# Kernel optimization log

Measured on AMD Instinct MI355X. Metric: run time of the kernel, lower is better.

Reference implementation:

```python
import jax, jax.numpy as jnp
import numpy as np

DIM = 16
HID = 32

def setup_inputs() -> dict:
    key = jax.random.key(0)
    ks = jax.random.split(key, 5)
    B, S = 32768, 64
    x = jax.random.normal(ks[0], (B, S, DIM), dtype=jnp.float32)
    # LayerNorm params (torch defaults: weight=1, bias=0)
    ln_w = jnp.ones((DIM,), dtype=jnp.float32)
    ln_b = jnp.zeros((DIM,), dtype=jnp.float32)
    # Linear params, torch-style init scale ~ 1/sqrt(fan_in)
    w1 = jax.random.uniform(ks[1], (HID, DIM), jnp.float32, -1.0, 1.0) / np.sqrt(DIM)
    b1 = jax.random.uniform(ks[2], (HID,), jnp.float32, -1.0, 1.0) / np.sqrt(DIM)
    w2 = jax.random.uniform(ks[3], (DIM, HID), jnp.float32, -1.0, 1.0) / np.sqrt(HID)
    b2 = jax.random.uniform(ks[4], (DIM,), jnp.float32, -1.0, 1.0) / np.sqrt(HID)
    return {"x": x, "ln_w": ln_w, "ln_b": ln_b, "w1": w1, "b1": b1, "w2": w2, "b2": b2}

def _layernorm(x, w, b, eps=1e-5):
    mu = jnp.mean(x, axis=-1, keepdims=True)
    var = jnp.mean(jnp.square(x - mu), axis=-1, keepdims=True)
    return (x - mu) * jax.lax.rsqrt(var + eps) * w + b

def reference(x, ln_w, ln_b, w1, b1, w2, b2):
    h = _layernorm(x, ln_w, ln_b)
    h = jnp.einsum('bsd,hd->bsh', h, w1) + b1
    h = jax.nn.gelu(h, approximate=False)  # torch nn.GELU default is exact erf
    h = jnp.einsum('bsh,dh->bsd', h, w2) + b2
    return x + h
```

## Files before the change

kernel.cpp:

```cpp
#include <hip/hip_runtime.h>
#include <math.h>

#define DIM 16
#define HID 32

typedef float  f32x4  __attribute__((ext_vector_type(4)));
typedef short  bf16x8 __attribute__((ext_vector_type(8)));
typedef float  v2f    __attribute__((ext_vector_type(2)));

#define ROW_STRIDE_B 80
#define LDS_PER_WAVE (64 * ROW_STRIDE_B)

__device__ inline unsigned short f2bf(float f) {
    union { float f; unsigned u; } v; v.f = f;
    unsigned r = v.u + 0x7fffu + ((v.u >> 16) & 1u);
    return (unsigned short)(r >> 16);
}
__device__ inline unsigned packbf(float lo, float hi) {
    return (unsigned)f2bf(lo) | ((unsigned)f2bf(hi) << 16);
}

__device__ inline float gelu_erf(float x) {
    const float kInvSqrt2 = 0.70710678118654752f;
    float z  = x * kInvSqrt2;
    float az = fabsf(z);
    float t  = __builtin_amdgcn_rcpf(fmaf(0.3275911f, az, 1.0f));
    float e  = __expf(-az * az);
    float p  = fmaf(t, 1.061405429f, -1.453152027f);
    p = fmaf(t, p, 1.421413741f);
    p = fmaf(t, p, -0.284496736f);
    p = fmaf(t, p, 0.254829592f);
    p = p * t;
    float erf_abs = fmaf(-p, e, 1.0f);
    float erfv = copysignf(erf_abs, z);
    return 0.5f * x * (1.0f + erfv);
}

__global__ __launch_bounds__(256) void fused_ln_mlp_mfma(
    const float* __restrict__ x,
    const float* __restrict__ ln_w,
    const float* __restrict__ ln_b,
    const float* __restrict__ w1,
    const float* __restrict__ b1,
    const float* __restrict__ w2,
    const float* __restrict__ b2,
    float* __restrict__ out,
    int nrows)
{
    __shared__ __align__(16) unsigned char lds_all[4 * LDS_PER_WAVE];

    const int tid  = threadIdx.x;
    const int lane = tid & 63;
    const int wave = tid >> 6;
    const int q    = lane >> 4;
    const int c    = lane & 15;

    unsigned char* nbuf = lds_all + wave * LDS_PER_WAVE;
    const int rowbase = (blockIdx.x * 4 + wave) * 64;

    bf16x8 bW1[2];
    #pragma unroll
    for (int t = 0; t < 2; t++) {
        bf16x8 f = {0, 0, 0, 0, 0, 0, 0, 0};
        if (q < 2) {
            const float* wp = w1 + (c + 16 * t) * DIM + q * 8;
            #pragma unroll
            for (int j = 0; j < 8; j++)
                ((unsigned short*)&f)[j] = f2bf(wp[j]);
        }
        bW1[t] = f;
    }
    bf16x8 bW2;
    {
        const float* wp = w2 + c * HID + q * 8;
        #pragma unroll
        for (int j = 0; j < 8; j++)
            ((unsigned short*)&bW2)[j] = f2bf(wp[j]);
    }
    const float b1v0 = b1[c];
    const float b1v1 = b1[c + 16];
    const float b2v  = b2[c];

    const float* xr = x + (size_t)(rowbase + lane) * DIM;
    v2f xv2[8];
    {
        float4 t0 = *(const float4*)(xr + 0);
        float4 t1 = *(const float4*)(xr + 4);
        float4 t2 = *(const float4*)(xr + 8);
        float4 t3 = *(const float4*)(xr + 12);
        xv2[0] = (v2f){t0.x, t0.y}; xv2[1] = (v2f){t0.z, t0.w};
        xv2[2] = (v2f){t1.x, t1.y}; xv2[3] = (v2f){t1.z, t1.w};
        xv2[4] = (v2f){t2.x, t2.y}; xv2[5] = (v2f){t2.z, t2.w};
        xv2[6] = (v2f){t3.x, t3.y}; xv2[7] = (v2f){t3.z, t3.w};
    }
    v2f s = xv2[0] + xv2[1];
    s += xv2[2] + xv2[3];
    s += xv2[4] + xv2[5];
    s += xv2[6] + xv2[7];
    float mu = (s.x + s.y) * (1.0f / DIM);
    v2f mu2 = (v2f){mu, mu};
    v2f vs = (v2f){0.0f, 0.0f};
    #pragma unroll
    for (int i = 0; i < 8; i++) {
        v2f d = xv2[i] - mu2;
        vs = __builtin_elementwise_fma(d, d, vs);
    }
    float var = (vs.x + vs.y) * (1.0f / DIM);
    float a = __builtin_amdgcn_rsqf(var + 1e-5f);
    float cc = -mu * a;

    const v2f* lnw2 = (const v2f*)ln_w;
    const v2f* lnb2 = (const v2f*)ln_b;
    v2f a2 = (v2f){a, a};
    v2f c2 = (v2f){cc, cc};
    float xn[16];
    #pragma unroll
    for (int i = 0; i < 8; i++) {
        v2f xh = __builtin_elementwise_fma(xv2[i], a2, c2);
        v2f r  = __builtin_elementwise_fma(xh, lnw2[i], lnb2[i]);
        xn[2 * i]     = r.x;
        xn[2 * i + 1] = r.y;
    }

    {
        int4 w0, w1v, zz;
        w0.x  = packbf(xn[0],  xn[1]);  w0.y  = packbf(xn[2],  xn[3]);
        w0.z  = packbf(xn[4],  xn[5]);  w0.w  = packbf(xn[6],  xn[7]);
        w1v.x = packbf(xn[8],  xn[9]);  w1v.y = packbf(xn[10], xn[11]);
        w1v.z = packbf(xn[12], xn[13]); w1v.w = packbf(xn[14], xn[15]);
        zz.x = zz.y = zz.z = zz.w = 0;
        int4* rowp = (int4*)(nbuf + lane * ROW_STRIDE_B);
        rowp[0] = w0; rowp[1] = w1v; rowp[2] = zz; rowp[3] = zz;
    }
    asm volatile("s_waitcnt lgkmcnt(0)" ::: "memory");

    f32x4 accH[4][2];
    #pragma unroll
    for (int rc = 0; rc < 4; rc++) {
        const bf16x8 afrag =
            *(const bf16x8*)(nbuf + (rc * 16 + c) * ROW_STRIDE_B + q * 16);
        f32x4 z0 = {0.f, 0.f, 0.f, 0.f};
        f32x4 z1 = {0.f, 0.f, 0.f, 0.f};
        accH[rc][0] = __builtin_amdgcn_mfma_f32_16x16x32_bf16(afrag, bW1[0], z0, 0, 0, 0);
        accH[rc][1] = __builtin_amdgcn_mfma_f32_16x16x32_bf16(afrag, bW1[1], z1, 0, 0, 0);
    }
    asm volatile("s_waitcnt lgkmcnt(0)" ::: "memory");

    #pragma unroll
    for (int rc = 0; rc < 4; rc++) {
        #pragma unroll
        for (int t = 0; t < 2; t++) {
            #pragma unroll
            for (int r = 0; r < 4; r++) {
                float hv = accH[rc][t][r] + (t ? b1v1 : b1v0);
                float g  = gelu_erf(hv);
                *(unsigned short*)(nbuf + (rc * 16 + 4 * q + r) * ROW_STRIDE_B
                                        + (c + 16 * t) * 2) = f2bf(g);
            }
        }
    }
    asm volatile("s_waitcnt lgkmcnt(0)" ::: "memory");

    f32x4 accY[4];
    #pragma unroll
    for (int rc = 0; rc < 4; rc++) {
        const bf16x8 afrag =
            *(const bf16x8*)(nbuf + (rc * 16 + c) * ROW_STRIDE_B + q * 16);
        f32x4 z = {0.f, 0.f, 0.f, 0.f};
        accY[rc] = __builtin_amdgcn_mfma_f32_16x16x32_bf16(afrag, bW2, z, 0, 0, 0);
    }

    #pragma unroll
    for (int rc = 0; rc < 4; rc++) {
        #pragma unroll
        for (int r = 0; r < 4; r++) {
            int grow = rowbase + rc * 16 + 4 * q + r;
            float xres = x[(size_t)grow * DIM + c];
            out[(size_t)grow * DIM + c] = accY[rc][r] + b2v + xres;
        }
    }
}

extern "C" void kernel_launch(void* const* d_in, const int* in_sizes, int n_in,
                              void* d_out, int out_size, void* d_ws, size_t ws_size,
                              hipStream_t stream) {
    const float* x    = (const float*)d_in[0];
    const float* ln_w = (const float*)d_in[1];
    const float* ln_b = (const float*)d_in[2];
    const float* w1   = (const float*)d_in[3];
    const float* b1   = (const float*)d_in[4];
    const float* w2   = (const float*)d_in[5];
    const float* b2   = (const float*)d_in[6];
    float* out = (float*)d_out;

    int nrows = in_sizes[0] / DIM;
    int rows_per_block = 256;
    int grid = (nrows + rows_per_block - 1) / rows_per_block;

    fused_ln_mlp_mfma<<<grid, 256, 0, stream>>>(
        x, ln_w, ln_b, w1, b1, w2, b2, out, nrows);
}
```

Before: 254.3 us.

## Transpose MFMA operands for row-major outputs, vectorize GELU, bf16 packing and stores

Swaps the MFMA operand order so each lane's accumulator holds four consecutive hidden or output columns of a single row. This lets the GELU results be written to LDS as packed int2 stores and the residual read and output write use 16-byte vector accesses with nontemporal stores, in place of scalar scattered ones. It also replaces software bf16 rounding with the hardware v_cvt_pk_bf16_f32 instruction and rewrites GELU in packed two-wide form using exp2 directly. One LDS barrier stage is removed by fusing GELU into the first MFMA loop. The inline asm relies on the conversion instruction existing on this target.

```diff
diff --git a/kernel.cpp b/kernel.cpp
--- a/kernel.cpp
+++ b/kernel.cpp
@@ -16,24 +16,31 @@
     unsigned r = v.u + 0x7fffu + ((v.u >> 16) & 1u);
     return (unsigned short)(r >> 16);
 }
-__device__ inline unsigned packbf(float lo, float hi) {
-    return (unsigned)f2bf(lo) | ((unsigned)f2bf(hi) << 16);
+
+__device__ inline unsigned cvt_pk_bf16(float lo, float hi) {
+    unsigned r;
+    asm("v_cvt_pk_bf16_f32 %0, %1, %2" : "=v"(r) : "v"(lo), "v"(hi));
+    return r;
 }
 
-__device__ inline float gelu_erf(float x) {
-    const float kInvSqrt2 = 0.70710678118654752f;
-    float z  = x * kInvSqrt2;
-    float az = fabsf(z);
-    float t  = __builtin_amdgcn_rcpf(fmaf(0.3275911f, az, 1.0f));
-    float e  = __expf(-az * az);
-    float p  = fmaf(t, 1.061405429f, -1.453152027f);
-    p = fmaf(t, p, 1.421413741f);
-    p = fmaf(t, p, -0.284496736f);
-    p = fmaf(t, p, 0.254829592f);
+__device__ inline v2f gelu2(v2f h) {
+    v2f hh  = h * (v2f){0.5f, 0.5f};
+    v2f ahh = __builtin_elementwise_abs(hh);
+    v2f az  = ahh * (v2f){1.41421356237309505f, 1.41421356237309505f};
+    v2f den = __builtin_elementwise_fma(az, (v2f){0.3275911f, 0.3275911f},
+                                        (v2f){1.0f, 1.0f});
+    v2f t   = (v2f){__builtin_amdgcn_rcpf(den.x), __builtin_amdgcn_rcpf(den.y)};
+    v2f h2  = h * h;
+    v2f ex  = h2 * (v2f){-0.721347520444482f, -0.721347520444482f};
+    v2f e   = (v2f){__builtin_amdgcn_exp2f(ex.x), __builtin_amdgcn_exp2f(ex.y)};
+    v2f p   = __builtin_elementwise_fma(t, (v2f){1.061405429f, 1.061405429f},
+                                        (v2f){-1.453152027f, -1.453152027f});
+    p = __builtin_elementwise_fma(t, p, (v2f){1.421413741f, 1.421413741f});
+    p = __builtin_elementwise_fma(t, p, (v2f){-0.284496736f, -0.284496736f});
+    p = __builtin_elementwise_fma(t, p, (v2f){0.254829592f, 0.254829592f});
     p = p * t;
-    float erf_abs = fmaf(-p, e, 1.0f);
-    float erfv = copysignf(erf_abs, z);
-    return 0.5f * x * (1.0f + erfv);
+    v2f erfa = __builtin_elementwise_fma(-p, e, (v2f){1.0f, 1.0f});
+    return __builtin_elementwise_fma(ahh, erfa, hh);
 }
 
 __global__ __launch_bounds__(256) void fused_ln_mlp_mfma(
@@ -57,8 +64,9 @@
 
     unsigned char* nbuf = lds_all + wave * LDS_PER_WAVE;
     const int rowbase = (blockIdx.x * 4 + wave) * 64;
+    (void)nrows;
 
-    bf16x8 bW1[2];
+    bf16x8 aW1[2];
     #pragma unroll
     for (int t = 0; t < 2; t++) {
         bf16x8 f = {0, 0, 0, 0, 0, 0, 0, 0};
@@ -68,26 +76,26 @@
             for (int j = 0; j < 8; j++)
                 ((unsigned short*)&f)[j] = f2bf(wp[j]);
         }
-        bW1[t] = f;
+        aW1[t] = f;
     }
-    bf16x8 bW2;
+    bf16x8 aW2;
     {
         const float* wp = w2 + c * HID + q * 8;
         #pragma unroll
         for (int j = 0; j < 8; j++)
-            ((unsigned short*)&bW2)[j] = f2bf(wp[j]);
+            ((unsigned short*)&aW2)[j] = f2bf(wp[j]);
     }
-    const float b1v0 = b1[c];
-    const float b1v1 = b1[c + 16];
-    const float b2v  = b2[c];
+    const f32x4 b1v0 = *(const f32x4*)(b1 + 4 * q);
+    const f32x4 b1v1 = *(const f32x4*)(b1 + 16 + 4 * q);
+    const f32x4 b2v4 = *(const f32x4*)(b2 + 4 * q);
 
     const float* xr = x + (size_t)(rowbase + lane) * DIM;
     v2f xv2[8];
     {
-        float4 t0 = *(const float4*)(xr + 0);
-        float4 t1 = *(const float4*)(xr + 4);
-        float4 t2 = *(const float4*)(xr + 8);
-        float4 t3 = *(const float4*)(xr + 12);
+        f32x4 t0 = *(const f32x4*)(xr + 0);
+        f32x4 t1 = *(const f32x4*)(xr + 4);
+        f32x4 t2 = *(const f32x4*)(xr + 8);
+        f32x4 t3 = *(const f32x4*)(xr + 12);
         xv2[0] = (v2f){t0.x, t0.y}; xv2[1] = (v2f){t0.z, t0.w};
         xv2[2] = (v2f){t1.x, t1.y}; xv2[3] = (v2f){t1.z, t1.w};
         xv2[4] = (v2f){t2.x, t2.y}; xv2[5] = (v2f){t2.z, t2.w};
@@ -113,71 +121,59 @@
     const v2f* lnb2 = (const v2f*)ln_b;
     v2f a2 = (v2f){a, a};
     v2f c2 = (v2f){cc, cc};
-    float xn[16];
+    unsigned dw[8];
     #pragma unroll
     for (int i = 0; i < 8; i++) {
         v2f xh = __builtin_elementwise_fma(xv2[i], a2, c2);
         v2f r  = __builtin_elementwise_fma(xh, lnw2[i], lnb2[i]);
-        xn[2 * i]     = r.x;
-        xn[2 * i + 1] = r.y;
+        dw[i] = cvt_pk_bf16(r.x, r.y);
     }
 
     {
         int4 w0, w1v, zz;
-        w0.x  = packbf(xn[0],  xn[1]);  w0.y  = packbf(xn[2],  xn[3]);
-        w0.z  = packbf(xn[4],  xn[5]);  w0.w  = packbf(xn[6],  xn[7]);
-        w1v.x = packbf(xn[8],  xn[9]);  w1v.y = packbf(xn[10], xn[11]);
-        w1v.z = packbf(xn[12], xn[13]); w1v.w = packbf(xn[14], xn[15]);
+        w0.x  = (int)dw[0]; w0.y  = (int)dw[1]; w0.z  = (int)dw[2]; w0.w  = (int)dw[3];
+        w1v.x = (int)dw[4]; w1v.y = (int)dw[5]; w1v.z = (int)dw[6]; w1v.w = (int)dw[7];
         zz.x = zz.y = zz.z = zz.w = 0;
         int4* rowp = (int4*)(nbuf + lane * ROW_STRIDE_B);
         rowp[0] = w0; rowp[1] = w1v; rowp[2] = zz; rowp[3] = zz;
     }
     asm volatile("s_waitcnt lgkmcnt(0)" ::: "memory");
 
-    f32x4 accH[4][2];
     #pragma unroll
     for (int rc = 0; rc < 4; rc++) {
-        const bf16x8 afrag =
+        const bf16x8 xfrag =
             *(const bf16x8*)(nbuf + (rc * 16 + c) * ROW_STRIDE_B + q * 16);
-        f32x4 z0 = {0.f, 0.f, 0.f, 0.f};
-        f32x4 z1 = {0.f, 0.f, 0.f, 0.f};
-        accH[rc][0] = __builtin_amdgcn_mfma_f32_16x16x32_bf16(afrag, bW1[0], z0, 0, 0, 0);
-        accH[rc][1] = __builtin_amdgcn_mfma_f32_16x16x32_bf16(afrag, bW1[1], z1, 0, 0, 0);
+        f32x4 z = {0.f, 0.f, 0.f, 0.f};
+        f32x4 h0 = __builtin_amdgcn_mfma_f32_16x16x32_bf16(aW1[0], xfrag, z, 0, 0, 0);
+        f32x4 h1 = __builtin_amdgcn_mfma_f32_16x16x32_bf16(aW1[1], xfrag, z, 0, 0, 0);
+        h0 += b1v0;
+        h1 += b1v1;
+        v2f g0 = gelu2((v2f){h0.x, h0.y});
+        v2f g1 = gelu2((v2f){h0.z, h0.w});
+        v2f g2 = gelu2((v2f){h1.x, h1.y});
+        v2f g3 = gelu2((v2f){h1.z, h1.w});
+        unsigned d0 = cvt_pk_bf16(g0.x, g0.y);
+        unsigned d1 = cvt_pk_bf16(g1.x, g1.y);
+        unsigned d2 = cvt_pk_bf16(g2.x, g2.y);
+        unsigned d3 = cvt_pk_bf16(g3.x, g3.y);
+        unsigned char* prow = nbuf + (rc * 16 + c) * ROW_STRIDE_B;
+        int2 lo; lo.x = (int)d0; lo.y = (int)d1;
+        int2 hi; hi.x = (int)d2; hi.y = (int)d3;
+        *(int2*)(prow + 8 * q)      = lo;
+        *(int2*)(prow + 32 + 8 * q) = hi;
     }
     asm volatile("s_waitcnt lgkmcnt(0)" ::: "memory");
 
     #pragma unroll
     for (int rc = 0; rc < 4; rc++) {
-        #pragma unroll
-        for (int t = 0; t < 2; t++) {
-            #pragma unroll
-            for (int r = 0; r < 4; r++) {
-                float hv = accH[rc][t][r] + (t ? b1v1 : b1v0);
-                float g  = gelu_erf(hv);
-                *(unsigned short*)(nbuf + (rc * 16 + 4 * q + r) * ROW_STRIDE_B
-                                        + (c + 16 * t) * 2) = f2bf(g);
-            }
-        }
-    }
-    asm volatile("s_waitcnt lgkmcnt(0)" ::: "memory");
-
-    f32x4 accY[4];
-    #pragma unroll
-    for (int rc = 0; rc < 4; rc++) {
-        const bf16x8 afrag =
+        const bf16x8 pfrag =
             *(const bf16x8*)(nbuf + (rc * 16 + c) * ROW_STRIDE_B + q * 16);
         f32x4 z = {0.f, 0.f, 0.f, 0.f};
-        accY[rc] = __builtin_amdgcn_mfma_f32_16x16x32_bf16(afrag, bW2, z, 0, 0, 0);
-    }
-
-    #pragma unroll
-    for (int rc = 0; rc < 4; rc++) {
-        #pragma unroll
-        for (int r = 0; r < 4; r++) {
-            int grow = rowbase + rc * 16 + 4 * q + r;
-            float xres = x[(size_t)grow * DIM + c];
-            out[(size_t)grow * DIM + c] = accY[rc][r] + b2v + xres;
-        }
+        f32x4 y = __builtin_amdgcn_mfma_f32_16x16x32_bf16(aW2, pfrag, z, 0, 0, 0);
+        size_t base = (size_t)(rowbase + rc * 16 + c) * DIM + 4 * q;
+        f32x4 xres = *(const f32x4*)(x + base);
+        f32x4 o = y + b2v4 + xres;
+        __builtin_nontemporal_store(o, (f32x4*)(out + base));
     }
 }
 
```

After: 242.2 us. 1.05x faster.
